# Kernel optimization log

Measured on AMD Instinct MI355X. Metric: run time of the kernel, lower is better.

## Reference

```python
import jax, jax.numpy as jnp
import numpy as np
import math

ACCBLOCK = 32
SPLITS = 2


def _mam(x, w, accblock):
    """MAM fully-connected: block-accumulate products along K, then max+min over blocks.
    x: [M, K], w: [K, N]  ->  [M, N] = max_blk(partial) + min_blk(partial)
    Implemented as a scan over blocks with running max/min to avoid a [M, nblk, N] tensor.
    """
    M, K = x.shape
    N = w.shape[1]
    nblk = K // accblock
    assert nblk * accblock == K
    xb = x.reshape(M, nblk, accblock).transpose(1, 0, 2)  # [nblk, M, B]
    wb = w.reshape(nblk, accblock, N)                      # [nblk, B, N]
    big = jnp.asarray(jnp.finfo(x.dtype).max, x.dtype)

    def step(carry, blk):
        mx, mn = carry
        xi, wi = blk                      # [M, B], [B, N]
        s = xi @ wi                       # block partial sum [M, N]
        return (jnp.maximum(mx, s), jnp.minimum(mn, s)), None

    init = (jnp.full((M, N), -big, x.dtype), jnp.full((M, N), big, x.dtype))
    (mx, mn), _ = jax.lax.scan(step, init, (xb, wb))
    return mx + mn


def reference(x, weight, bias):
    # eval mode, vcon_steps=0 -> alpha=1, beta=0; no weight dropout, no output dropout
    in_features = weight.shape[1]
    w = weight.T  # [K, N]
    sub = math.ceil(in_features / SPLITS)
    last = in_features - sub * (SPLITS - 1)
    out = _mam(x[:, :sub], w[:sub], ACCBLOCK)
    for i in range(1, SPLITS - 1):
        out = out + _mam(x[:, i * sub:(i + 1) * sub], w[i * sub:(i + 1) * sub], ACCBLOCK)
    out = out + _mam(x[:, in_features - last:], w[in_features - last:], ACCBLOCK)
    return out + bias[None, :]


def setup_inputs() -> dict:
    key = jax.random.key(0)
    k1, k2, k3 = jax.random.split(key, 3)
    M, K, N = 2048, 4096, 4096
    x = jax.random.normal(k1, (M, K), dtype=jnp.float32)
    weight = jax.random.normal(k2, (N, K), dtype=jnp.float32) * (1.0 / math.sqrt(K))
    bias = jax.random.normal(k3, (N,), dtype=jnp.float32) * (1.0 / math.sqrt(K))
    return {"x": x, "weight": weight, "bias": bias}
```

## Files before the change

kernel.cpp:

```cpp
#include <hip/hip_runtime.h>
#include <cstdint>
#include <cstddef>

typedef __bf16 bf16;
typedef __bf16 bf16x4 __attribute__((ext_vector_type(4)));
typedef __bf16 bf16x8 __attribute__((ext_vector_type(8)));
typedef float  f32x4  __attribute__((ext_vector_type(4)));

#define MDIM 2048
#define NDIM 4096
#define KDIM 4096
#define FLOATMAX 3.402823466e38f

__global__ void cvt2_f32_to_bf16(const float* __restrict__ x, const float* __restrict__ w,
                                 bf16* __restrict__ xb, bf16* __restrict__ wb,
                                 int xn4, int wn4) {
    const int stride = gridDim.x * blockDim.x;
    int i = blockIdx.x * blockDim.x + threadIdx.x;
    for (int k = i; k < xn4; k += stride) {
        f32x4 v = reinterpret_cast<const f32x4*>(x)[k];
        reinterpret_cast<bf16x4*>(xb)[k] = __builtin_convertvector(v, bf16x4);
    }
    for (int k = i; k < wn4; k += stride) {
        f32x4 v = reinterpret_cast<const f32x4*>(w)[k];
        reinterpret_cast<bf16x4*>(wb)[k] = __builtin_convertvector(v, bf16x4);
    }
}

__device__ __forceinline__ void g2lds16(const bf16* g, bf16* l) {
    __builtin_amdgcn_global_load_lds(
        (const __attribute__((address_space(1))) uint32_t*)g,
        (__attribute__((address_space(3))) uint32_t*)l, 16, 0, 0);
}

__global__ __launch_bounds__(256) void mam_kernel(
    const bf16* __restrict__ A,
    const bf16* __restrict__ B,
    const float* __restrict__ bias,
    float* __restrict__ out)
{
    __shared__ __align__(16) bf16 sA[2][2][128 * 32];
    __shared__ __align__(16) bf16 sB[2][2][128 * 32];

    const int t    = threadIdx.x;
    const int lane = t & 63;
    const int w    = t >> 6;
    const int wm   = (w >> 1) * 64;
    const int wn   = (w & 1) * 64;

    const int m0 = blockIdx.y * 128;
    const int n0 = blockIdx.x * 128;

    const int srow   = t >> 2;
    const int spos   = t & 3;
    const int schunk = spos ^ ((srow >> 1) & 3);
    const bf16* gA = A + (size_t)(m0 + srow) * KDIM + schunk * 8;
    const bf16* gB = B + (size_t)(n0 + srow) * KDIM + schunk * 8;
    const int ldst = t * 8;

    const int frow = lane & 15;
    const int q    = lane >> 4;
    const int swz  = (q ^ ((frow >> 1) & 3)) * 8;
    const int offA0 = (wm + frow) * 32 + swz;
    const int offB0 = (wn + frow) * 32 + swz;

    const f32x4 kZero = {0.f, 0.f, 0.f, 0.f};

    f32x4 mx[4][4], mn[4][4];
#pragma unroll
    for (int i = 0; i < 4; ++i)
#pragma unroll
        for (int j = 0; j < 4; ++j) {
            mx[i][j] = (f32x4)(-FLOATMAX);
            mn[i][j] = (f32x4)(FLOATMAX);
        }

    auto prefetch = [&](int s, int pb) {
        const bf16* ga = gA + (size_t)s * 64;
        const bf16* gb = gB + (size_t)s * 64;
        g2lds16(ga,                  &sA[pb][0][ldst]);
        g2lds16(ga + 64 * KDIM,      &sA[pb][0][2048 + ldst]);
        g2lds16(ga + 32,             &sA[pb][1][ldst]);
        g2lds16(ga + 64 * KDIM + 32, &sA[pb][1][2048 + ldst]);
        g2lds16(gb,                  &sB[pb][0][ldst]);
        g2lds16(gb + 64 * KDIM,      &sB[pb][0][2048 + ldst]);
        g2lds16(gb + 32,             &sB[pb][1][ldst]);
        g2lds16(gb + 64 * KDIM + 32, &sB[pb][1][2048 + ldst]);
    };

    auto compute = [&](int pb) {
        bf16x8 bF0[4], bF1[4];
#pragma unroll
        for (int j = 0; j < 4; ++j) {
            bF0[j] = *(const bf16x8*)&sB[pb][0][offB0 + j * 512];
            bF1[j] = *(const bf16x8*)&sB[pb][1][offB0 + j * 512];
        }
#pragma unroll
        for (int i = 0; i < 4; ++i) {
            const bf16x8 a0 = *(const bf16x8*)&sA[pb][0][offA0 + i * 512];
            const bf16x8 a1 = *(const bf16x8*)&sA[pb][1][offA0 + i * 512];
#pragma unroll
            for (int j = 0; j < 4; ++j) {
                f32x4 s0 = __builtin_amdgcn_mfma_f32_16x16x32_bf16(
                    a0, bF0[j], kZero, 0, 0, 0);
                f32x4 s1 = __builtin_amdgcn_mfma_f32_16x16x32_bf16(
                    a1, bF1[j], kZero, 0, 0, 0);
#pragma unroll
                for (int r = 0; r < 4; ++r) {
                    mx[i][j][r] = fmaxf(fmaxf(mx[i][j][r], s0[r]), s1[r]);
                    mn[i][j][r] = fminf(fminf(mn[i][j][r], s0[r]), s1[r]);
                }
            }
        }
    };

    const int orow = (lane >> 4) * 4;
    const int ocol = lane & 15;

    prefetch(0, 0);

    int bb = 0;
#pragma unroll 1
    for (int it = 0; it < 16; ++it) {
        __syncthreads();
        prefetch(bb + 1, 1);
        compute(0);
        ++bb;
        __syncthreads();
        prefetch(bb + 1, 0);
        compute(1);
        ++bb;
    }

#pragma unroll
    for (int j = 0; j < 4; ++j) {
        const int col = n0 + wn + j * 16 + ocol;
#pragma unroll
        for (int i = 0; i < 4; ++i) {
            const int row = m0 + wm + i * 16 + orow;
#pragma unroll
            for (int r = 0; r < 4; ++r)
                out[(size_t)(row + r) * NDIM + col] = mx[i][j][r] + mn[i][j][r];
            mx[i][j] = (f32x4)(-FLOATMAX);
            mn[i][j] = (f32x4)(FLOATMAX);
        }
    }

#pragma unroll 1
    for (int it = 0; it < 16; ++it) {
        __syncthreads();
        prefetch(bb + 1, 1);
        compute(0);
        ++bb;
        __syncthreads();
        if (bb < 63) prefetch(bb + 1, 0);
        compute(1);
        ++bb;
    }

#pragma unroll
    for (int j = 0; j < 4; ++j) {
        const int col = n0 + wn + j * 16 + ocol;
        const float bv = bias[col];
#pragma unroll
        for (int i = 0; i < 4; ++i) {
            const int row = m0 + wm + i * 16 + orow;
#pragma unroll
            for (int r = 0; r < 4; ++r) {
                const size_t idx = (size_t)(row + r) * NDIM + col;
                out[idx] = out[idx] + (mx[i][j][r] + mn[i][j][r]) + bv;
            }
        }
    }
}

extern "C" void kernel_launch(void* const* d_in, const int* in_sizes, int n_in,
                              void* d_out, int out_size, void* d_ws, size_t ws_size,
                              hipStream_t stream) {
    const float* x    = (const float*)d_in[0];
    const float* wgt  = (const float*)d_in[1];
    const float* bias = (const float*)d_in[2];
    float* out = (float*)d_out;

    bf16* xbf = (bf16*)d_ws;
    bf16* wbf = xbf + (size_t)MDIM * KDIM;

    const int xn4 = (MDIM * KDIM) / 4;
    const int wn4 = (NDIM * KDIM) / 4;
    cvt2_f32_to_bf16<<<dim3(4096), dim3(256), 0, stream>>>(x, wgt, xbf, wbf, xn4, wn4);

    dim3 grid(NDIM / 128, MDIM / 128);
    mam_kernel<<<grid, dim3(256), 0, stream>>>(xbf, wbf, bias, out);
}
```

Baseline: 314.7 us.

## Deepen LDS pipeline to four stages with vmcnt waits and remap tiles

Replaces the double-buffered 64-wide K staging with a 4-deep ring of 32-wide K stages. Each step prefetches three stages ahead and waits with an explicit s_waitcnt vmcnt plus a raw s_barrier instead of __syncthreads, so global-to-LDS loads stay in flight across iterations. The two split loops are merged into a single 128-step loop that writes the first-split result at the midpoint. Block indices are also remapped so that groups of workgroups share A/B tiles for better L2 reuse. The cost is more barriers per unit of K and fragile hand-tuned wait counts.

```diff
diff --git a/kernel.cpp b/kernel.cpp
--- a/kernel.cpp
+++ b/kernel.cpp
@@ -33,14 +33,16 @@
         (__attribute__((address_space(3))) uint32_t*)l, 16, 0, 0);
 }
 
+#define WAITVM(N) asm volatile("s_waitcnt vmcnt(" #N ")" ::: "memory")
+
 __global__ __launch_bounds__(256) void mam_kernel(
     const bf16* __restrict__ A,
     const bf16* __restrict__ B,
     const float* __restrict__ bias,
     float* __restrict__ out)
 {
-    __shared__ __align__(16) bf16 sA[2][2][128 * 32];
-    __shared__ __align__(16) bf16 sB[2][2][128 * 32];
+    __shared__ __align__(16) bf16 sA[4][128 * 32];
+    __shared__ __align__(16) bf16 sB[4][128 * 32];
 
     const int t    = threadIdx.x;
     const int lane = t & 63;
@@ -48,8 +50,10 @@
     const int wm   = (w >> 1) * 64;
     const int wn   = (w & 1) * 64;
 
-    const int m0 = blockIdx.y * 128;
-    const int n0 = blockIdx.x * 128;
+    const int lin    = blockIdx.x + blockIdx.y * gridDim.x;
+    const int newlin = (lin & 7) * 64 + (lin >> 3);
+    const int m0 = (newlin >> 5) * 128;
+    const int n0 = (newlin & 31) * 128;
 
     const int srow   = t >> 2;
     const int spos   = t & 3;
@@ -75,40 +79,33 @@
             mn[i][j] = (f32x4)(FLOATMAX);
         }
 
-    auto prefetch = [&](int s, int pb) {
-        const bf16* ga = gA + (size_t)s * 64;
-        const bf16* gb = gB + (size_t)s * 64;
-        g2lds16(ga,                  &sA[pb][0][ldst]);
-        g2lds16(ga + 64 * KDIM,      &sA[pb][0][2048 + ldst]);
-        g2lds16(ga + 32,             &sA[pb][1][ldst]);
-        g2lds16(ga + 64 * KDIM + 32, &sA[pb][1][2048 + ldst]);
-        g2lds16(gb,                  &sB[pb][0][ldst]);
-        g2lds16(gb + 64 * KDIM,      &sB[pb][0][2048 + ldst]);
-        g2lds16(gb + 32,             &sB[pb][1][ldst]);
-        g2lds16(gb + 64 * KDIM + 32, &sB[pb][1][2048 + ldst]);
+    auto prefetch = [&](int s) {
+        const int buf = s & 3;
+        const bf16* ga = gA + (size_t)s * 32;
+        const bf16* gb = gB + (size_t)s * 32;
+        g2lds16(ga,                  &sA[buf][ldst]);
+        g2lds16(ga + 64 * KDIM,      &sA[buf][2048 + ldst]);
+        g2lds16(gb,                  &sB[buf][ldst]);
+        g2lds16(gb + 64 * KDIM,      &sB[buf][2048 + ldst]);
     };
 
-    auto compute = [&](int pb) {
-        bf16x8 bF0[4], bF1[4];
+    auto compute = [&](int s) {
+        const int buf = s & 3;
+        bf16x8 bF[4];
 #pragma unroll
-        for (int j = 0; j < 4; ++j) {
-            bF0[j] = *(const bf16x8*)&sB[pb][0][offB0 + j * 512];
-            bF1[j] = *(const bf16x8*)&sB[pb][1][offB0 + j * 512];
-        }
+        for (int j = 0; j < 4; ++j)
+            bF[j] = *(const bf16x8*)&sB[buf][offB0 + j * 512];
 #pragma unroll
         for (int i = 0; i < 4; ++i) {
-            const bf16x8 a0 = *(const bf16x8*)&sA[pb][0][offA0 + i * 512];
-            const bf16x8 a1 = *(const bf16x8*)&sA[pb][1][offA0 + i * 512];
+            const bf16x8 a = *(const bf16x8*)&sA[buf][offA0 + i * 512];
 #pragma unroll
             for (int j = 0; j < 4; ++j) {
-                f32x4 s0 = __builtin_amdgcn_mfma_f32_16x16x32_bf16(
-                    a0, bF0[j], kZero, 0, 0, 0);
-                f32x4 s1 = __builtin_amdgcn_mfma_f32_16x16x32_bf16(
-                    a1, bF1[j], kZero, 0, 0, 0);
+                f32x4 sv = __builtin_amdgcn_mfma_f32_16x16x32_bf16(
+                    a, bF[j], kZero, 0, 0, 0);
 #pragma unroll
                 for (int r = 0; r < 4; ++r) {
-                    mx[i][j][r] = fmaxf(fmaxf(mx[i][j][r], s0[r]), s1[r]);
-                    mn[i][j][r] = fminf(fminf(mn[i][j][r], s0[r]), s1[r]);
+                    mx[i][j][r] = fmaxf(mx[i][j][r], sv[r]);
+                    mn[i][j][r] = fminf(mn[i][j][r], sv[r]);
                 }
             }
         }
@@ -117,45 +114,41 @@
     const int orow = (lane >> 4) * 4;
     const int ocol = lane & 15;
 
-    prefetch(0, 0);
-
-    int bb = 0;
-#pragma unroll 1
-    for (int it = 0; it < 16; ++it) {
-        __syncthreads();
-        prefetch(bb + 1, 1);
-        compute(0);
-        ++bb;
-        __syncthreads();
-        prefetch(bb + 1, 0);
-        compute(1);
-        ++bb;
-    }
-
-#pragma unroll
-    for (int j = 0; j < 4; ++j) {
-        const int col = n0 + wn + j * 16 + ocol;
-#pragma unroll
-        for (int i = 0; i < 4; ++i) {
-            const int row = m0 + wm + i * 16 + orow;
-#pragma unroll
-            for (int r = 0; r < 4; ++r)
-                out[(size_t)(row + r) * NDIM + col] = mx[i][j][r] + mn[i][j][r];
-            mx[i][j] = (f32x4)(-FLOATMAX);
-            mn[i][j] = (f32x4)(FLOATMAX);
-        }
-    }
+    prefetch(0);
+    prefetch(1);
+    prefetch(2);
+    WAITVM(8);
+    __builtin_amdgcn_s_barrier();
+    __builtin_amdgcn_sched_barrier(0);
 
 #pragma unroll 1
-    for (int it = 0; it < 16; ++it) {
-        __syncthreads();
-        prefetch(bb + 1, 1);
-        compute(0);
-        ++bb;
-        __syncthreads();
-        if (bb < 63) prefetch(bb + 1, 0);
-        compute(1);
-        ++bb;
+    for (int s = 0; s < 128; ++s) {
+        if (s + 3 < 128) prefetch(s + 3);
+        compute(s);
+
+        if (s == 63) {
+#pragma unroll
+            for (int j = 0; j < 4; ++j) {
+                const int col = n0 + wn + j * 16 + ocol;
+#pragma unroll
+                for (int i = 0; i < 4; ++i) {
+                    const int row = m0 + wm + i * 16 + orow;
+#pragma unroll
+                    for (int r = 0; r < 4; ++r)
+                        out[(size_t)(row + r) * NDIM + col] = mx[i][j][r] + mn[i][j][r];
+                    mx[i][j] = (f32x4)(-FLOATMAX);
+                    mn[i][j] = (f32x4)(FLOATMAX);
+                }
+            }
+        }
+
+        if (s < 127) {
+            if (s < 125)       { WAITVM(8); }
+            else if (s == 125) { WAITVM(4); }
+            else               { WAITVM(0); }
+            __builtin_amdgcn_s_barrier();
+            __builtin_amdgcn_sched_barrier(0);
+        }
     }
 
 #pragma unroll
```

Measured after the change: 372.1 us. 1.18x slower.
